# Kernel optimization log

Hardware: AMD Instinct MI355X
Metric: run time of the kernel (lower is better)

Reference implementation:

```python
import jax, jax.numpy as jnp
import numpy as np

D_MODEL = 1024
N_HEADS = 16
D_K = D_MODEL // N_HEADS


def setup_inputs() -> dict:
    key = jax.random.key(0)
    ks = jax.random.split(key, 7)
    B, S, D = 2, 2048, D_MODEL
    scale = 1.0 / np.sqrt(D)
    return {
        "query": jax.random.normal(ks[0], (B, S, D), dtype=jnp.float32),
        "key": jax.random.normal(ks[1], (B, S, D), dtype=jnp.float32),
        "value": jax.random.normal(ks[2], (B, S, D), dtype=jnp.float32),
        "w_q": jax.random.normal(ks[3], (D, D), dtype=jnp.float32) * scale,
        "w_k": jax.random.normal(ks[4], (D, D), dtype=jnp.float32) * scale,
        "w_v": jax.random.normal(ks[5], (D, D), dtype=jnp.float32) * scale,
        "w_o": jax.random.normal(ks[6], (D, D), dtype=jnp.float32) * scale,
    }


def reference(query, key, value, w_q, w_k, w_v, w_o):
    B, S, D = query.shape
    H, Dk = N_HEADS, D_K
    # nn.Linear (no bias): x @ W.T ; then split heads -> [B, H, S, Dk]
    def split_heads(x, W):
        return (x @ W.T).reshape(B, S, H, Dk).transpose(0, 2, 1, 3)
    Q = split_heads(query, w_q)
    K = split_heads(key, w_k)
    V = split_heads(value, w_v)
    scores = jnp.einsum("bhqd,bhkd->bhqk", Q, K) / np.sqrt(Dk).astype(jnp.float32)
    attn = jax.nn.softmax(scores, axis=-1)  # dropout is identity in eval
    attended = jnp.einsum("bhqk,bhkd->bhqd", attn, V)
    attended = attended.transpose(0, 2, 1, 3).reshape(B, S, D)
    output = attended @ w_o.T
    avg_attention = attn.mean(axis=1)  # mean over heads -> [B, S, S]
    return (output, avg_attention)
```

## Files before the change

kernel.cpp:

```cpp
#include <hip/hip_runtime.h>
#include <math.h>

#define SEQ 2048
#define DMODEL 1024
#define NH 16
#define DK 64
#define BATCH 2

using bf16x8 = __attribute__((ext_vector_type(8))) __bf16;
using bf16x4 = __attribute__((ext_vector_type(4))) __bf16;
using f32x4  = __attribute__((ext_vector_type(4))) float;

__device__ inline f32x4 mfma16(bf16x8 a, bf16x8 b, f32x4 c) {
    return __builtin_amdgcn_mfma_f32_16x16x32_bf16(a, b, c, 0, 0, 0);
}

__device__ inline void load_lds16(const void* g, void* l) {
    __builtin_amdgcn_global_load_lds(
        (const __attribute__((address_space(1))) void*)g,
        (__attribute__((address_space(3))) void*)l, 16, 0, 0);
}

#define VMCNT(n) asm volatile("s_waitcnt vmcnt(" #n ")" ::: "memory")
#define BARRIER() __builtin_amdgcn_s_barrier()
#define CFENCE() asm volatile("" ::: "memory")
#define EXP_SCALE 0.18033688011112042f
#define EXP2(x) __builtin_amdgcn_exp2f(x)

__global__ __launch_bounds__(256) void conv_bf16(
        const float* __restrict__ q, const float* __restrict__ k,
        const float* __restrict__ v, const float* __restrict__ wq,
        const float* __restrict__ wk, const float* __restrict__ wv,
        const float* __restrict__ wo,
        __bf16* __restrict__ oq, __bf16* __restrict__ ok, __bf16* __restrict__ ov,
        __bf16* __restrict__ owq, __bf16* __restrict__ owk,
        __bf16* __restrict__ owv, __bf16* __restrict__ owo) {
    int bid = blockIdx.x;
    const float* src;
    __bf16* dst;
    size_t off;
    if (bid < 3072) {
        int ti = bid >> 10;
        src = ti == 0 ? q : (ti == 1 ? k : v);
        dst = ti == 0 ? oq : (ti == 1 ? ok : ov);
        off = (size_t)(bid & 1023) * 4096;
    } else {
        int ti = (bid - 3072) >> 8;
        src = ti == 0 ? wq : (ti == 1 ? wk : (ti == 2 ? wv : wo));
        dst = ti == 0 ? owq : (ti == 1 ? owk : (ti == 2 ? owv : owo));
        off = (size_t)((bid - 3072) & 255) * 4096;
    }
    src += off; dst += off;
    const int t = threadIdx.x;
#pragma unroll
    for (int i = 0; i < 4; ++i) {
        float4 x = *(const float4*)(src + t * 4 + i * 1024);
        bf16x4 y;
        y[0] = (__bf16)x.x; y[1] = (__bf16)x.y;
        y[2] = (__bf16)x.z; y[3] = (__bf16)x.w;
        *(bf16x4*)(dst + t * 4 + i * 1024) = y;
    }
}

__device__ __forceinline__ void gemm_core(const __bf16* __restrict__ A,
                                          const __bf16* __restrict__ B,
                                          void* __restrict__ out, int mode,
                                          int m0, int n0, int N,
                                          __bf16* As, __bf16* Bs) {
    const int t    = threadIdx.x;
    const int w    = t >> 6;
    const int lane = t & 63;
    const int m    = lane & 15;
    const int kg   = lane >> 4;
    const int wr   = w >> 1, wc = w & 1;

    auto stage = [&](int buf, int k0) {
        const __bf16* ga0 = A + (size_t)(m0 + w * 16 + m) * 1024 + k0 + kg * 8;
        load_lds16(ga0, &As[buf * 4096 + w * 512]);
        const __bf16* ga1 = A + (size_t)(m0 + (w + 4) * 16 + m) * 1024 + k0 + kg * 8;
        load_lds16(ga1, &As[buf * 4096 + (w + 4) * 512]);
        const __bf16* gb0 = B + (size_t)(n0 + w * 16 + m) * 1024 + k0 + kg * 8;
        load_lds16(gb0, &Bs[buf * 4096 + w * 512]);
        const __bf16* gb1 = B + (size_t)(n0 + (w + 4) * 16 + m) * 1024 + k0 + kg * 8;
        load_lds16(gb1, &Bs[buf * 4096 + (w + 4) * 512]);
    };

    f32x4 acc[4][4] = {};

    stage(0, 0);
    CFENCE();
    stage(1, 32);

    int cb = 0, sb = 2;
    for (int ts = 0; ts < 32; ++ts) {
        if (ts < 30) {
            stage(sb, (ts + 2) * 32);
            VMCNT(8);
        } else if (ts == 30) {
            VMCNT(4);
        } else {
            VMCNT(0);
        }
        BARRIER();
        CFENCE();
        const __bf16* Ac = &As[cb * 4096];
        const __bf16* Bc = &Bs[cb * 4096];
        bf16x8 af[4], bg[4];
#pragma unroll
        for (int i = 0; i < 4; ++i)
            af[i] = *(const bf16x8*)&Ac[(wr * 4 + i) * 512 + lane * 8];
#pragma unroll
        for (int j = 0; j < 4; ++j)
            bg[j] = *(const bf16x8*)&Bc[(wc * 4 + j) * 512 + lane * 8];
        __builtin_amdgcn_s_setprio(1);
#pragma unroll
        for (int i = 0; i < 4; ++i)
#pragma unroll
            for (int j = 0; j < 4; ++j)
                acc[i][j] = mfma16(af[i], bg[j], acc[i][j]);
        __builtin_amdgcn_s_setprio(0);
        BARRIER();
        cb = cb == 2 ? 0 : cb + 1;
        sb = sb == 2 ? 0 : sb + 1;
    }

#pragma unroll
    for (int i = 0; i < 4; ++i) {
        const int rb = m0 + wr * 64 + i * 16 + kg * 4;
#pragma unroll
        for (int j = 0; j < 4; ++j) {
            const int gc = n0 + wc * 64 + j * 16 + m;
#pragma unroll
            for (int r = 0; r < 4; ++r) {
                const int gr = rb + r;
                const float vv = acc[i][j][r];
                if (mode == 0) {
                    ((float*)out)[(size_t)gr * N + gc] = vv;
                } else if (mode == 1) {
                    ((__bf16*)out)[(size_t)gr * N + gc] = (__bf16)vv;
                } else {
                    const int hh = gr >> 6, dd = gr & 63;
                    const int bb = gc >> 11, ss = gc & 2047;
                    ((__bf16*)out)[(((size_t)bb * NH + hh) * DK + dd) * SEQ + ss] = (__bf16)vv;
                }
            }
        }
    }
}

__device__ __forceinline__ int xcd_swz(int s, int cpx) {
    return (s & 7) * cpx + (s >> 3);
}

__global__ __launch_bounds__(256, 3) void gemm_qkv(
        const __bf16* __restrict__ Xq, const __bf16* __restrict__ Wq, __bf16* Qr,
        const __bf16* __restrict__ Xk, const __bf16* __restrict__ Wk, __bf16* Kr,
        const __bf16* __restrict__ Xv, const __bf16* __restrict__ Wv, __bf16* Vt) {
    __shared__ __align__(16) __bf16 As[12288];
    __shared__ __align__(16) __bf16 Bs[12288];
    const int bid = blockIdx.x;
    if (bid < 256) {
        const int s = xcd_swz(bid, 32);
        gemm_core(Xq, Wq, Qr, 1, (s >> 3) * 128, (s & 7) * 128, 1024, As, Bs);
    } else if (bid < 512) {
        const int s = xcd_swz(bid - 256, 32);
        gemm_core(Xk, Wk, Kr, 1, (s >> 3) * 128, (s & 7) * 128, 1024, As, Bs);
    } else {
        const int s = xcd_swz(bid - 512, 32);
        gemm_core(Wv, Xv, Vt, 2, (s >> 5) * 128, (s & 31) * 128, 4096, As, Bs);
    }
}

__global__ __launch_bounds__(512, 4) void attn_flash(const __bf16* __restrict__ Qr,
                                                     const __bf16* __restrict__ Kr,
                                                     const __bf16* __restrict__ Vt,
                                                     __bf16* __restrict__ att,
                                                     float* __restrict__ invs) {
    __shared__ __align__(16) unsigned char smem[66048];
    __bf16* Ks   = (__bf16*)smem;
    __bf16* Vs   = (__bf16*)(smem + 16384);
    __bf16* Pb   = (__bf16*)(smem + 32768);
    float*  sinv = (float*)(smem + 65536);

    const int t    = threadIdx.x;
    const int w    = t >> 6;
    const int lane = t & 63;
    const int m    = lane & 15;
    const int kg   = lane >> 4;

    const int L  = xcd_swz(blockIdx.x, 64);
    const int b  = L >> 8;
    const int h  = (L >> 4) & 15;
    const int qw = (L & 15) * 128 + w * 16;

    const __bf16* Kh = Kr + (size_t)b * SEQ * 1024 + h * 64;
    const __bf16* Vh = Vt + ((size_t)b * NH + h) * DK * SEQ;
    __bf16* Pw = Pb + w * 2048;

    const size_t rowQ = (size_t)(b * SEQ + qw + m) * 1024 + h * 64 + kg * 8;
    const bf16x8 qa = *(const bf16x8*)(Qr + rowQ);
    const bf16x8 qb = *(const bf16x8*)(Qr + rowQ + 32);

    const int rk0 = t >> 3,          ck0 = t & 7;
    const int rk1 = (t + 512) >> 3,  ck1 = (t + 512) & 7;
    const int rv0 = t >> 4,          cv0 = t & 15;
    const int rv1 = (t + 512) >> 4,  cv1 = (t + 512) & 15;
    bf16x8 kst0, kst1, vst0, vst1;

    auto issue = [&](int kt) {
        kst0 = *(const bf16x8*)(Kh + (size_t)(kt + rk0) * 1024 + ck0 * 8);
        kst1 = *(const bf16x8*)(Kh + (size_t)(kt + rk1) * 1024 + ck1 * 8);
        vst0 = *(const bf16x8*)(Vh + (size_t)rv0 * SEQ + kt + cv0 * 8);
        vst1 = *(const bf16x8*)(Vh + (size_t)rv1 * SEQ + kt + cv1 * 8);
    };
    auto commit = [&]() {
        *(bf16x8*)&Ks[rk0 * 64 + ((ck0 ^ (rk0 & 7)) * 8)] = kst0;
        *(bf16x8*)&Ks[rk1 * 64 + ((ck1 ^ (rk1 & 7)) * 8)] = kst1;
        *(bf16x8*)&Vs[rv0 * 128 + ((cv0 ^ (rv0 & 7)) * 8)] = vst0;
        *(bf16x8*)&Vs[rv1 * 128 + ((cv1 ^ (rv1 & 7)) * 8)] = vst1;
    };

    f32x4 pv[4] = {};
    float rsum = 0.f;

    issue(0);
    commit();
    __syncthreads();

    for (int kt = 0; kt < SEQ; kt += 128) {
        if (kt + 128 < SEQ) issue(kt + 128);
#pragma unroll
        for (int nt = 0; nt < 8; ++nt) {
            const int row = nt * 16 + m;
            bf16x8 k0 = *(const bf16x8*)&Ks[row * 64 + ((kg ^ (m & 7)) * 8)];
            bf16x8 k1 = *(const bf16x8*)&Ks[row * 64 + (((kg + 4) ^ (m & 7)) * 8)];
            f32x4 c = {};
            c = mfma16(k0, qa, c);
            c = mfma16(k1, qb, c);
            bf16x4 pk;
#pragma unroll
            for (int r = 0; r < 4; ++r) {
                float p = EXP2(c[r] * EXP_SCALE);
                rsum += p;
                pk[r] = (__bf16)p;
            }
            const int up = (nt * 2 + (kg >> 1)) ^ (m & 7);
            *(bf16x4*)&Pw[m * 128 + (((up << 1) | (kg & 1)) * 4)] = pk;
        }
#pragma unroll
        for (int ks = 0; ks < 4; ++ks) {
            const int u = (ks * 4 + kg) ^ (m & 7);
            bf16x8 pa = *(const bf16x8*)&Pw[m * 128 + u * 8];
#pragma unroll
            for (int nt = 0; nt < 4; ++nt) {
                const int rv = nt * 16 + m;
                bf16x8 vb = *(const bf16x8*)&Vs[rv * 128 + u * 8];
                pv[nt] = mfma16(pa, vb, pv[nt]);
            }
        }
        __syncthreads();
        if (kt + 128 < SEQ) {
            commit();
            asm volatile("s_waitcnt lgkmcnt(0)" ::: "memory");
            BARRIER();
        }
    }

    rsum += __shfl_xor(rsum, 16);
    rsum += __shfl_xor(rsum, 32);
    const float inv = 1.0f / rsum;
    if (lane < 16) {
        sinv[w * 16 + m] = inv;
        invs[((size_t)b * NH + h) * SEQ + qw + m] = inv;
    }
    __syncthreads();
    float iv[4];
#pragma unroll
    for (int r = 0; r < 4; ++r) iv[r] = sinv[w * 16 + kg * 4 + r];

    float* scf = (float*)smem + w * 1088;
#pragma unroll
    for (int nt = 0; nt < 4; ++nt)
#pragma unroll
        for (int r = 0; r < 4; ++r)
            scf[(kg * 4 + r) * 68 + nt * 16 + m] = pv[nt][r] * iv[r];
    __syncthreads();
    {
        const int q = lane >> 2, c0 = (lane & 3) * 16;
        const float* srcf = &scf[q * 68 + c0];
        bf16x8 o0, o1;
#pragma unroll
        for (int j = 0; j < 8; ++j) {
            o0[j] = (__bf16)srcf[j];
            o1[j] = (__bf16)srcf[j + 8];
        }
        __bf16* dst = att + (size_t)(b * SEQ + qw + q) * DMODEL + h * DK + c0;
        *(bf16x8*)(dst)     = o0;
        *(bf16x8*)(dst + 8) = o1;
    }
}

__device__ __forceinline__ void avg_core(const __bf16* __restrict__ Qr,
                                         const __bf16* __restrict__ Kr,
                                         const float* __restrict__ invs,
                                         float* __restrict__ avg,
                                         int L, __bf16* Kb) {
    const int t    = threadIdx.x;
    const int w    = t >> 6;
    const int lane = t & 63;
    const int m    = lane & 15;
    const int kg   = lane >> 4;
    const int b    = L >> 9;
    const int s0   = ((L >> 5) & 15) * 128;
    const int qw   = (L & 31) * 64 + w * 16;

    const __bf16* Kbase = Kr + (size_t)(b * SEQ + s0) * 1024;

    auto stageK = [&](int buf, int h) {
#pragma unroll
        for (int s = 0; s < 4; ++s) {
            const int i   = w * 4 + s;
            const int row = i * 8 + (lane >> 3);
            const int u   = lane & 7;
            load_lds16(Kbase + (size_t)row * 1024 + h * 64 + ((u ^ (row & 7)) * 8),
                       Kb + buf * 8192 + i * 512);
        }
    };

    f32x4 acc[8] = {};

    stageK(0, 0);
    const size_t qoff = (size_t)(b * SEQ + qw + m) * 1024 + kg * 8;
    bf16x8 a0 = *(const bf16x8*)(Qr + qoff);
    bf16x8 a1 = *(const bf16x8*)(Qr + qoff + 32);
    f32x4 ivr = *(const f32x4*)&invs[(size_t)b * NH * SEQ + qw + kg * 4];
    __syncthreads();

    int cur = 0;
    for (int h = 0; h < NH; ++h) {
        if (h + 1 < NH) stageK(cur ^ 1, h + 1);
        bf16x8 na0, na1;
        f32x4 nivr;
        if (h + 1 < NH) {
            na0  = *(const bf16x8*)(Qr + qoff + (h + 1) * 64);
            na1  = *(const bf16x8*)(Qr + qoff + (h + 1) * 64 + 32);
            nivr = *(const f32x4*)&invs[((size_t)b * NH + h + 1) * SEQ + qw + kg * 4];
        }
        const __bf16* Kc = Kb + cur * 8192;
#pragma unroll
        for (int nt = 0; nt < 8; ++nt) {
            const int row = nt * 16 + m;
            bf16x8 k0 = *(const bf16x8*)&Kc[row * 64 + ((kg ^ (m & 7)) * 8)];
            bf16x8 k1 = *(const bf16x8*)&Kc[row * 64 + (((kg + 4) ^ (m & 7)) * 8)];
            f32x4 c = {};
            c = mfma16(a0, k0, c);
            c = mfma16(a1, k1, c);
#pragma unroll
            for (int r = 0; r < 4; ++r)
                acc[nt][r] += ivr[r] * EXP2(c[r] * EXP_SCALE);
        }
        __syncthreads();
        cur ^= 1;
        a0 = na0; a1 = na1; ivr = nivr;
    }

    const float sc = 1.0f / NH;
#pragma unroll
    for (int nt = 0; nt < 8; ++nt)
#pragma unroll
        for (int r = 0; r < 4; ++r)
            avg[(size_t)(b * SEQ + qw + kg * 4 + r) * SEQ + s0 + nt * 16 + m] =
                acc[nt][r] * sc;
}

__global__ __launch_bounds__(256, 3) void gemm_wo_avg(
        const __bf16* __restrict__ At, const __bf16* __restrict__ Wo,
        float* __restrict__ out,
        const __bf16* __restrict__ Qr, const __bf16* __restrict__ Kr,
        const float* __restrict__ invs, float* __restrict__ avg) {
    __shared__ __align__(16) __bf16 sm[24576];
    const int bid = blockIdx.x;
    if (bid < 256) {
        const int s = xcd_swz(bid, 32);
        gemm_core(At, Wo, out, 0, (s >> 3) * 128, (s & 7) * 128, 1024,
                  sm, sm + 12288);
    } else {
        avg_core(Qr, Kr, invs, avg, xcd_swz(bid - 256, 128), sm);
    }
}

extern "C" void kernel_launch(void* const* d_in, const int* in_sizes, int n_in,
                              void* d_out, int out_size, void* d_ws, size_t ws_size,
                              hipStream_t stream) {
    const float* query = (const float*)d_in[0];
    const float* key   = (const float*)d_in[1];
    const float* value = (const float*)d_in[2];
    const float* w_q   = (const float*)d_in[3];
    const float* w_k   = (const float*)d_in[4];
    const float* w_v   = (const float*)d_in[5];
    const float* w_o   = (const float*)d_in[6];

    float* out = (float*)d_out;
    float* avg = out + (size_t)BATCH * SEQ * DMODEL;

    __bf16* Xq = (__bf16*)d_ws;
    __bf16* Xk = Xq + 4194304;
    __bf16* Xv = Xk + 4194304;
    __bf16* Wq = Xv + 4194304;
    __bf16* Wk = Wq + 1048576;
    __bf16* Wv = Wk + 1048576;
    __bf16* Wo = Wv + 1048576;
    __bf16* Qr = Wo + 1048576;
    __bf16* Kr = Qr + 4194304;
    __bf16* Vt = Kr + 4194304;
    float*  Invs = (float*)(Vt + 4194304);
    __bf16* At = Xq;

    conv_bf16<<<4096, 256, 0, stream>>>(query, key, value, w_q, w_k, w_v, w_o,
                                        Xq, Xk, Xv, Wq, Wk, Wv, Wo);

    gemm_qkv<<<768, 256, 0, stream>>>(Xq, Wq, Qr, Xk, Wk, Kr, Xv, Wv, Vt);

    attn_flash<<<512, 512, 0, stream>>>(Qr, Kr, Vt, At, Invs);

    gemm_wo_avg<<<1280, 256, 0, stream>>>(At, Wo, out, Qr, Kr, Invs, avg);
}
```

Baseline: 263.6 us.

## Restructure flash attention with async LDS double-buffering and register-resident P

Attention blocks shrink to 256 threads over 64 queries, doubling the grid. K/V tiles of 64 keys are now staged straight into LDS with global_load_lds in an MFMA-fragment-friendly order and double-buffered with vmcnt waits, replacing the register-staged load/commit. The key permutation lets the probability tile stay in registers as the A operand of the PV MFMA, removing the P round trip through LDS. The avg kernel's K staging uses the same fragment layout. The risk is more barriers per key and fewer waves per block to hide latency.

```diff
diff --git a/kernel.cpp b/kernel.cpp
--- a/kernel.cpp
+++ b/kernel.cpp
@@ -171,16 +171,14 @@
     }
 }
 
-__global__ __launch_bounds__(512, 4) void attn_flash(const __bf16* __restrict__ Qr,
+__global__ __launch_bounds__(256, 4) void attn_flash(const __bf16* __restrict__ Qr,
                                                      const __bf16* __restrict__ Kr,
                                                      const __bf16* __restrict__ Vt,
                                                      __bf16* __restrict__ att,
                                                      float* __restrict__ invs) {
-    __shared__ __align__(16) unsigned char smem[66048];
-    __bf16* Ks   = (__bf16*)smem;
-    __bf16* Vs   = (__bf16*)(smem + 16384);
-    __bf16* Pb   = (__bf16*)(smem + 32768);
-    float*  sinv = (float*)(smem + 65536);
+    __shared__ __align__(16) unsigned char smem[32768];
+    __bf16* Kb = (__bf16*)smem;
+    __bf16* Vb = Kb + 8192;
 
     const int t    = threadIdx.x;
     const int w    = t >> 6;
@@ -188,87 +186,89 @@
     const int m    = lane & 15;
     const int kg   = lane >> 4;
 
-    const int L  = xcd_swz(blockIdx.x, 64);
-    const int b  = L >> 8;
-    const int h  = (L >> 4) & 15;
-    const int qw = (L & 15) * 128 + w * 16;
+    const int L  = xcd_swz(blockIdx.x, 128);
+    const int b  = L >> 9;
+    const int h  = (L >> 5) & 15;
+    const int qw = (L & 31) * 64 + w * 16;
 
     const __bf16* Kh = Kr + (size_t)b * SEQ * 1024 + h * 64;
     const __bf16* Vh = Vt + ((size_t)b * NH + h) * DK * SEQ;
-    __bf16* Pw = Pb + w * 2048;
 
     const size_t rowQ = (size_t)(b * SEQ + qw + m) * 1024 + h * 64 + kg * 8;
     const bf16x8 qa = *(const bf16x8*)(Qr + rowQ);
     const bf16x8 qb = *(const bf16x8*)(Qr + rowQ + 32);
-
-    const int rk0 = t >> 3,          ck0 = t & 7;
-    const int rk1 = (t + 512) >> 3,  ck1 = (t + 512) & 7;
-    const int rv0 = t >> 4,          cv0 = t & 15;
-    const int rv1 = (t + 512) >> 4,  cv1 = (t + 512) & 15;
-    bf16x8 kst0, kst1, vst0, vst1;
-
-    auto issue = [&](int kt) {
-        kst0 = *(const bf16x8*)(Kh + (size_t)(kt + rk0) * 1024 + ck0 * 8);
-        kst1 = *(const bf16x8*)(Kh + (size_t)(kt + rk1) * 1024 + ck1 * 8);
-        vst0 = *(const bf16x8*)(Vh + (size_t)rv0 * SEQ + kt + cv0 * 8);
-        vst1 = *(const bf16x8*)(Vh + (size_t)rv1 * SEQ + kt + cv1 * 8);
+    CFENCE();
+
+    auto kaddr = [&](int bk, int kt) {
+        const int p = bk >> 1, dh = bk & 1, i = lane & 15;
+        const int key = (p >> 1) * 32 + ((i >> 2) * 8) + (p & 1) * 4 + (i & 3);
+        return (const void*)(Kh + (size_t)(kt + key) * 1024 + dh * 32 + (lane >> 4) * 8);
     };
-    auto commit = [&]() {
-        *(bf16x8*)&Ks[rk0 * 64 + ((ck0 ^ (rk0 & 7)) * 8)] = kst0;
-        *(bf16x8*)&Ks[rk1 * 64 + ((ck1 ^ (rk1 & 7)) * 8)] = kst1;
-        *(bf16x8*)&Vs[rv0 * 128 + ((cv0 ^ (rv0 & 7)) * 8)] = vst0;
-        *(bf16x8*)&Vs[rv1 * 128 + ((cv1 ^ (rv1 & 7)) * 8)] = vst1;
+    auto vaddr = [&](int bk, int kt) {
+        const int nt = bk >> 1, kv = bk & 1, i = lane & 15;
+        return (const void*)(Vh + (size_t)(nt * 16 + i) * SEQ + kt + kv * 32 + (lane >> 4) * 8);
+    };
+    auto stage = [&](int buf, int kt) {
+        load_lds16(kaddr(w, kt),     Kb + buf * 4096 + w * 512);
+        load_lds16(kaddr(w + 4, kt), Kb + buf * 4096 + (w + 4) * 512);
+        load_lds16(vaddr(w, kt),     Vb + buf * 4096 + w * 512);
+        load_lds16(vaddr(w + 4, kt), Vb + buf * 4096 + (w + 4) * 512);
     };
 
     f32x4 pv[4] = {};
     float rsum = 0.f;
 
-    issue(0);
-    commit();
-    __syncthreads();
-
-    for (int kt = 0; kt < SEQ; kt += 128) {
-        if (kt + 128 < SEQ) issue(kt + 128);
-#pragma unroll
-        for (int nt = 0; nt < 8; ++nt) {
-            const int row = nt * 16 + m;
-            bf16x8 k0 = *(const bf16x8*)&Ks[row * 64 + ((kg ^ (m & 7)) * 8)];
-            bf16x8 k1 = *(const bf16x8*)&Ks[row * 64 + (((kg + 4) ^ (m & 7)) * 8)];
+    stage(0, 0);
+    CFENCE();
+    stage(1, 64);
+
+    int cur = 0;
+    for (int ts = 0; ts < 32; ++ts) {
+        if (ts < 31) { VMCNT(4); } else { VMCNT(0); }
+        BARRIER();
+        CFENCE();
+        const __bf16* Kc = Kb + cur * 4096;
+        const __bf16* Vc = Vb + cur * 4096;
+        bf16x4 pk[4];
+#pragma unroll
+        for (int p = 0; p < 4; ++p) {
+            bf16x8 k0 = *(const bf16x8*)&Kc[(p * 2 + 0) * 512 + lane * 8];
+            bf16x8 k1 = *(const bf16x8*)&Kc[(p * 2 + 1) * 512 + lane * 8];
             f32x4 c = {};
             c = mfma16(k0, qa, c);
             c = mfma16(k1, qb, c);
-            bf16x4 pk;
+            bf16x4 t4;
 #pragma unroll
             for (int r = 0; r < 4; ++r) {
-                float p = EXP2(c[r] * EXP_SCALE);
-                rsum += p;
-                pk[r] = (__bf16)p;
+                float pe = EXP2(c[r] * EXP_SCALE);
+                rsum += pe;
+                t4[r] = (__bf16)pe;
             }
-            const int up = (nt * 2 + (kg >> 1)) ^ (m & 7);
-            *(bf16x4*)&Pw[m * 128 + (((up << 1) | (kg & 1)) * 4)] = pk;
-        }
-#pragma unroll
-        for (int ks = 0; ks < 4; ++ks) {
-            const int u = (ks * 4 + kg) ^ (m & 7);
-            bf16x8 pa = *(const bf16x8*)&Pw[m * 128 + u * 8];
+            pk[p] = t4;
+        }
+#pragma unroll
+        for (int ks = 0; ks < 2; ++ks) {
+            bf16x8 pa;
+#pragma unroll
+            for (int e = 0; e < 4; ++e) {
+                pa[e]     = pk[2 * ks][e];
+                pa[4 + e] = pk[2 * ks + 1][e];
+            }
 #pragma unroll
             for (int nt = 0; nt < 4; ++nt) {
-                const int rv = nt * 16 + m;
-                bf16x8 vb = *(const bf16x8*)&Vs[rv * 128 + u * 8];
+                bf16x8 vb = *(const bf16x8*)&Vc[(nt * 2 + ks) * 512 + lane * 8];
                 pv[nt] = mfma16(pa, vb, pv[nt]);
             }
         }
-        __syncthreads();
-        if (kt + 128 < SEQ) {
-            commit();
-            asm volatile("s_waitcnt lgkmcnt(0)" ::: "memory");
-            BARRIER();
-        }
+        BARRIER();
+        if (ts + 2 < 32) stage(cur, (ts + 2) * 64);
+        cur ^= 1;
     }
 
     rsum += __shfl_xor(rsum, 16);
     rsum += __shfl_xor(rsum, 32);
     const float inv = 1.0f / rsum;
+    float* sinv = (float*)(smem + 17408);
     if (lane < 16) {
         sinv[w * 16 + m] = inv;
         invs[((size_t)b * NH + h) * SEQ + qw + m] = inv;
@@ -319,11 +319,11 @@
     auto stageK = [&](int buf, int h) {
 #pragma unroll
         for (int s = 0; s < 4; ++s) {
-            const int i   = w * 4 + s;
-            const int row = i * 8 + (lane >> 3);
-            const int u   = lane & 7;
-            load_lds16(Kbase + (size_t)row * 1024 + h * 64 + ((u ^ (row & 7)) * 8),
-                       Kb + buf * 8192 + i * 512);
+            const int bk = w * 4 + s;
+            const int nt = bk >> 1, dh = bk & 1;
+            load_lds16(Kbase + (size_t)(nt * 16 + (lane & 15)) * 1024 + h * 64 +
+                           dh * 32 + (lane >> 4) * 8,
+                       Kb + buf * 8192 + bk * 512);
         }
     };
 
@@ -349,9 +349,8 @@
         const __bf16* Kc = Kb + cur * 8192;
 #pragma unroll
         for (int nt = 0; nt < 8; ++nt) {
-            const int row = nt * 16 + m;
-            bf16x8 k0 = *(const bf16x8*)&Kc[row * 64 + ((kg ^ (m & 7)) * 8)];
-            bf16x8 k1 = *(const bf16x8*)&Kc[row * 64 + (((kg + 4) ^ (m & 7)) * 8)];
+            bf16x8 k0 = *(const bf16x8*)&Kc[(nt * 2 + 0) * 512 + lane * 8];
+            bf16x8 k1 = *(const bf16x8*)&Kc[(nt * 2 + 1) * 512 + lane * 8];
             f32x4 c = {};
             c = mfma16(a0, k0, c);
             c = mfma16(a1, k1, c);
@@ -421,7 +420,7 @@
 
     gemm_qkv<<<768, 256, 0, stream>>>(Xq, Wq, Qr, Xk, Wk, Kr, Xv, Wv, Vt);
 
-    attn_flash<<<512, 512, 0, stream>>>(Qr, Kr, Vt, At, Invs);
+    attn_flash<<<1024, 256, 0, stream>>>(Qr, Kr, Vt, At, Invs);
 
     gemm_wo_avg<<<1280, 256, 0, stream>>>(At, Wo, out, Qr, Kr, Invs, avg);
 }
```

Result: slower. 293.8 us (+11.5%).
